# Kernel tuning notes

Hardware: AMD Instinct MI355X
Metric: run time of the kernel (lower is better)

The kernel has to match this reference:

```python
import jax, jax.numpy as jnp
import numpy as np

I, H, O, L = 256, 512, 256, 2
B, S = 64, 512


def setup_inputs() -> dict:
    key = jax.random.key(0)
    ks = jax.random.split(key, 10)
    s_in = 1.0 / np.sqrt(I)
    s_h = 1.0 / np.sqrt(H)
    return {
        "x": jax.random.normal(ks[0], (B, S, I), dtype=jnp.float32),
        "h_prev": jnp.zeros((L, B, H), dtype=jnp.float32),
        "W_in": jax.random.uniform(ks[1], (I, H), jnp.float32, -s_in, s_in),
        "b_in": jax.random.uniform(ks[2], (H,), jnp.float32, -s_in, s_in),
        "W_i2h": jax.random.uniform(ks[3], (L, H, H), jnp.float32, -s_h, s_h),
        "b_i2h": jax.random.uniform(ks[4], (L, H), jnp.float32, -s_h, s_h),
        "W_h2h": jax.random.uniform(ks[5], (L, H, H), jnp.float32, -s_h, s_h),
        "b_h2h": jax.random.uniform(ks[6], (L, H), jnp.float32, -s_h, s_h),
        "W_out": jax.random.uniform(ks[7], (H, O), jnp.float32, -s_h, s_h),
        "b_out": jax.random.uniform(ks[8], (O,), jnp.float32, -s_h, s_h),
    }


def reference(x, h_prev, W_in, b_in, W_i2h, b_i2h, W_h2h, b_h2h, W_out, b_out):
    # x: [B, S, I]; h_prev: [L, B, H]
    def step(h, x_t):  # h: [L,B,H], x_t: [B,I]
        layer_in = x_t @ W_in + b_in  # [B,H]
        new_hs = []
        for l in range(L):
            h_l = jnp.tanh(layer_in @ W_i2h[l] + b_i2h[l] + h[l] @ W_h2h[l] + b_h2h[l])
            new_hs.append(h_l)
            layer_in = h_l
        h_new = jnp.stack(new_hs, axis=0)  # [L,B,H]
        out_t = layer_in @ W_out + b_out  # [B,O]
        return h_new, out_t

    xs = jnp.swapaxes(x, 0, 1)  # [S,B,I]
    h_t, outs = jax.lax.scan(step, h_prev, xs)
    outputs = jnp.swapaxes(outs, 0, 1)  # [B,S,O]
    return outputs, h_t
```

## Files before the change

### kernel.cpp

```cpp
#include <hip/hip_runtime.h>
#include <math.h>


constexpr int BB = 64;
constexpr int SS = 512;
constexpr int II = 256;
constexpr int HH = 512;
constexpr int OO = 256;
constexpr int BH = BB * HH;
constexpr int RING_D = 4;
constexpr int STR0 = 772;
constexpr int STR1 = 1028;
constexpr int PSTR = 36;
constexpr int HREG = 8 * STR1;
constexpr int PREG = 8 * 32 * PSTR;
constexpr int LDS_BYTES = (HREG + PREG) * 4;

#define SCOPE_AGENT __HIP_MEMORY_SCOPE_AGENT

__device__ __forceinline__ unsigned ld_flag(const unsigned* p) {
    return __hip_atomic_load((unsigned*)p, __ATOMIC_RELAXED, SCOPE_AGENT);
}
__device__ __forceinline__ void add_flag(unsigned* p) {
    __hip_atomic_fetch_add(p, 1u, __ATOMIC_RELAXED, SCOPE_AGENT);
}
__device__ __forceinline__ void wait_ge(const unsigned* p, unsigned target) {
    while (ld_flag(p) < target) __builtin_amdgcn_s_sleep(1);
}

union F2U { float2 f; unsigned long long u; };
__device__ __forceinline__ float2 ld_coh2(const float* p) {
    F2U v;
    v.u = __hip_atomic_load((unsigned long long*)p, __ATOMIC_RELAXED, SCOPE_AGENT);
    return v.f;
}
__device__ __forceinline__ void st_coh1(float* p, float a) {
    __hip_atomic_store(p, a, __ATOMIC_RELAXED, SCOPE_AGENT);
}

template <int N>
__device__ __forceinline__ void pin4(float4 (&w)[N]) {
    #pragma unroll
    for (int i = 0; i < N; ++i)
        asm volatile("" : "+v"(w[i].x), "+v"(w[i].y), "+v"(w[i].z), "+v"(w[i].w));
}

__global__ __launch_bounds__(256) void fold_k(
    const float* __restrict__ Win, const float* __restrict__ bin,
    const float* __restrict__ Wi2h, const float* __restrict__ bi2h,
    const float* __restrict__ bh2h,
    float* __restrict__ W0, float* __restrict__ b0)
{
    int gid = blockIdx.x * 256 + threadIdx.x;
    const float* Wi0 = Wi2h;
    if (gid < II * HH) {
        int i = gid / HH, j = gid % HH;
        float acc = 0.f;
        for (int k = 0; k < HH; ++k)
            acc = fmaf(Win[i * HH + k], Wi0[k * HH + j], acc);
        W0[gid] = acc;
    } else if (gid < II * HH + HH) {
        int j = gid - II * HH;
        float acc = bi2h[j] + bh2h[j];
        for (int k = 0; k < HH; ++k)
            acc = fmaf(bin[k], Wi0[k * HH + j], acc);
        b0[j] = acc;
    }
}

template <int LAYER>
__device__ __forceinline__ void rnn_body(
    const float* __restrict__ x, const float* __restrict__ hprev,
    const float* __restrict__ Wi2h, const float* __restrict__ bi2h,
    const float* __restrict__ Wh2h, const float* __restrict__ bh2h,
    const float* __restrict__ W0, const float* __restrict__ b0,
    float* __restrict__ ring, float* __restrict__ H1,
    unsigned* __restrict__ c0, unsigned* __restrict__ c1,
    float* hbuf, float* pbuf)
{
    constexpr int NJ  = LAYER ? 8 : 6;
    constexpr int STR = LAYER ? STR1 : STR0;

    const int tid  = threadIdx.x;
    const int id   = blockIdx.x & 127;
    const int rg   = id >> 4;
    const int cg   = id & 15;
    const int row0 = rg * 8;
    const int col0 = cg * 32;
    const int kg   = tid & 31;
    const int cgrp = (tid >> 5) & 7;
    const int cbase = col0 + cgrp * 4;

    float4 w4[NJ * 4];
    #pragma unroll
    for (int j = 0; j < NJ; ++j) {
        #pragma unroll
        for (int e = 0; e < 4; ++e) {
            int k = j * 128 + kg * 4 + e;
            const float* src;
            if (LAYER == 0)
                src = (k < 512) ? (Wh2h + (size_t)k * HH + cbase)
                                : (W0 + (size_t)(k - 512) * HH + cbase);
            else
                src = (k < 512) ? (Wi2h + (size_t)HH * HH + (size_t)k * HH + cbase)
                                : (Wh2h + (size_t)HH * HH + (size_t)(k - 512) * HH + cbase);
            w4[j * 4 + e] = *(const float4*)src;
        }
    }
    pin4(w4);

    float bias_red;
    {
        int c = col0 + (tid & 31);
        bias_red = LAYER ? (bi2h[HH + c] + bh2h[HH + c]) : b0[c];
    }
    const int rr = tid >> 5, cl = tid & 31;

    for (int t = 0; t < SS; ++t) {
        if (tid == 0) {
            if (LAYER == 0) {
                if (t >= 1) wait_ge(c0 + rg, 16u * (unsigned)t);
                if (t >= RING_D) wait_ge(c1 + rg, 16u * (unsigned)(t - RING_D + 1));
            } else {
                wait_ge(c0 + rg, 16u * (unsigned)(t + 1));
                if (t >= 1) wait_ge(c1 + rg, 16u * (unsigned)t);
            }
        }
        __syncthreads();

        if (LAYER == 0) {
            const float* hsrc = (t == 0)
                ? (hprev + (size_t)row0 * HH)
                : (ring + (size_t)((t - 1) & (RING_D - 1)) * BH + (size_t)row0 * HH);
            float2 tmp[8];
            #pragma unroll
            for (int u = 0; u < 8; ++u) tmp[u] = ld_coh2(hsrc + u * HH + 2 * tid);
            float4 xv[2];
            #pragma unroll
            for (int v = 0; v < 2; ++v) {
                int rx = 4 * v + (tid >> 6);
                xv[v] = *(const float4*)(x + ((size_t)(row0 + rx) * SS + t) * II + 4 * (tid & 63));
            }
            #pragma unroll
            for (int u = 0; u < 8; ++u) *(float2*)&hbuf[u * STR + 2 * tid] = tmp[u];
            #pragma unroll
            for (int v = 0; v < 2; ++v) {
                int rx = 4 * v + (tid >> 6);
                *(float4*)&hbuf[rx * STR + 512 + 4 * (tid & 63)] = xv[v];
            }
        } else {
            const float* h0src = ring + (size_t)(t & (RING_D - 1)) * BH + (size_t)row0 * HH;
            const float* h1src = (t == 0)
                ? (hprev + BH + (size_t)row0 * HH)
                : (H1 + (size_t)(t - 1) * BH + (size_t)row0 * HH);
            float2 ta[8], tb[8];
            #pragma unroll
            for (int u = 0; u < 8; ++u) ta[u] = ld_coh2(h0src + u * HH + 2 * tid);
            #pragma unroll
            for (int u = 0; u < 8; ++u) tb[u] = ld_coh2(h1src + u * HH + 2 * tid);
            #pragma unroll
            for (int u = 0; u < 8; ++u) *(float2*)&hbuf[u * STR + 2 * tid] = ta[u];
            #pragma unroll
            for (int u = 0; u < 8; ++u) *(float2*)&hbuf[u * STR + 512 + 2 * tid] = tb[u];
        }
        __syncthreads();

        float4 acc[8];
        #pragma unroll
        for (int r = 0; r < 8; ++r) acc[r] = make_float4(0.f, 0.f, 0.f, 0.f);
        #pragma unroll
        for (int r = 0; r < 8; ++r) {
            #pragma unroll
            for (int j = 0; j < NJ; ++j) {
                float4 h4 = *(const float4*)&hbuf[r * STR + j * 128 + kg * 4];
                float4 wa = w4[j * 4 + 0];
                float4 wb = w4[j * 4 + 1];
                float4 wc = w4[j * 4 + 2];
                float4 wd = w4[j * 4 + 3];
                acc[r].x = fmaf(h4.x, wa.x, acc[r].x);
                acc[r].y = fmaf(h4.x, wa.y, acc[r].y);
                acc[r].z = fmaf(h4.x, wa.z, acc[r].z);
                acc[r].w = fmaf(h4.x, wa.w, acc[r].w);
                acc[r].x = fmaf(h4.y, wb.x, acc[r].x);
                acc[r].y = fmaf(h4.y, wb.y, acc[r].y);
                acc[r].z = fmaf(h4.y, wb.z, acc[r].z);
                acc[r].w = fmaf(h4.y, wb.w, acc[r].w);
                acc[r].x = fmaf(h4.z, wc.x, acc[r].x);
                acc[r].y = fmaf(h4.z, wc.y, acc[r].y);
                acc[r].z = fmaf(h4.z, wc.z, acc[r].z);
                acc[r].w = fmaf(h4.z, wc.w, acc[r].w);
                acc[r].x = fmaf(h4.w, wd.x, acc[r].x);
                acc[r].y = fmaf(h4.w, wd.y, acc[r].y);
                acc[r].z = fmaf(h4.w, wd.z, acc[r].z);
                acc[r].w = fmaf(h4.w, wd.w, acc[r].w);
            }
        }

        #pragma unroll
        for (int r = 0; r < 8; ++r) {
            pbuf[(r * 32 + cgrp * 4 + 0) * PSTR + kg] = acc[r].x;
            pbuf[(r * 32 + cgrp * 4 + 1) * PSTR + kg] = acc[r].y;
            pbuf[(r * 32 + cgrp * 4 + 2) * PSTR + kg] = acc[r].z;
            pbuf[(r * 32 + cgrp * 4 + 3) * PSTR + kg] = acc[r].w;
        }
        __syncthreads();
        {
            float s = 0.f;
            #pragma unroll
            for (int j2 = 0; j2 < 8; ++j2) {
                float4 v = *(const float4*)&pbuf[(rr * 32 + cl) * PSTR + 4 * j2];
                s += (v.x + v.y) + (v.z + v.w);
            }
            float o = tanhf(s + bias_red);
            float* dst = LAYER
                ? (H1 + (size_t)t * BH + (size_t)(row0 + rr) * HH + col0 + cl)
                : (ring + (size_t)(t & (RING_D - 1)) * BH + (size_t)(row0 + rr) * HH + col0 + cl);
            st_coh1(dst, o);
        }
        __syncthreads();
        if (tid == 0) add_flag((LAYER ? c1 : c0) + rg);
    }
}

__global__ __launch_bounds__(256, 1) void rnn_seq6(
    const float* __restrict__ x, const float* __restrict__ hprev,
    const float* __restrict__ Wi2h, const float* __restrict__ bi2h,
    const float* __restrict__ Wh2h, const float* __restrict__ bh2h,
    const float* __restrict__ W0, const float* __restrict__ b0,
    float* __restrict__ ring, float* __restrict__ H1,
    unsigned* __restrict__ c0, unsigned* __restrict__ c1)
{
    extern __shared__ float lds[];
    float* hbuf = lds;
    float* pbuf = lds + HREG;
    if (blockIdx.x >> 7)
        rnn_body<1>(x, hprev, Wi2h, bi2h, Wh2h, bh2h, W0, b0, ring, H1, c0, c1, hbuf, pbuf);
    else
        rnn_body<0>(x, hprev, Wi2h, bi2h, Wh2h, bh2h, W0, b0, ring, H1, c0, c1, hbuf, pbuf);
}

__global__ __launch_bounds__(256) void out_k(
    const float* __restrict__ H1, const float* __restrict__ Wout,
    const float* __restrict__ bout, float* __restrict__ out)
{
    __shared__ float wchunk[32 * 256];
    __shared__ float htile[16 * 32];
    const int tid = threadIdx.x;
    const int r0 = blockIdx.x * 16;

    float acc[16];
    #pragma unroll
    for (int mm = 0; mm < 16; ++mm) acc[mm] = 0.f;

    for (int kc = 0; kc < HH; kc += 32) {
        for (int idx = tid; idx < 32 * 256; idx += 256)
            wchunk[idx] = Wout[(size_t)(kc + (idx >> 8)) * OO + (idx & 255)];
        for (int idx = tid; idx < 16 * 32; idx += 256) {
            int mm = idx >> 5, kk = idx & 31;
            htile[idx] = H1[(size_t)(r0 + mm) * HH + kc + kk];
        }
        __syncthreads();
        for (int kk = 0; kk < 32; ++kk) {
            float w = wchunk[kk * 256 + tid];
            #pragma unroll
            for (int mm = 0; mm < 16; ++mm)
                acc[mm] = fmaf(htile[mm * 32 + kk], w, acc[mm]);
        }
        __syncthreads();
    }
    float bo = bout[tid];
    #pragma unroll
    for (int mm = 0; mm < 16; ++mm) {
        int rr = r0 + mm;
        int s = rr >> 6, b = rr & 63;
        out[((size_t)b * SS + s) * OO + tid] = acc[mm] + bo;
    }
}

__global__ __launch_bounds__(256) void tail_k(
    const float* __restrict__ ring, const float* __restrict__ H1,
    float* __restrict__ out_tail)
{
    int gid = blockIdx.x * 256 + threadIdx.x;
    if (gid < BB * HH)
        out_tail[gid] = ring[((SS - 1) & (RING_D - 1)) * BH + gid];
    else if (gid < 2 * BB * HH)
        out_tail[gid] = H1[(size_t)(SS - 1) * BH + (gid - BB * HH)];
}

extern "C" void kernel_launch(void* const* d_in, const int* in_sizes, int n_in,
                              void* d_out, int out_size, void* d_ws, size_t ws_size,
                              hipStream_t stream)
{
    const float* x     = (const float*)d_in[0];
    const float* hprev = (const float*)d_in[1];
    const float* Win   = (const float*)d_in[2];
    const float* bin   = (const float*)d_in[3];
    const float* Wi2h  = (const float*)d_in[4];
    const float* bi2h  = (const float*)d_in[5];
    const float* Wh2h  = (const float*)d_in[6];
    const float* bh2h  = (const float*)d_in[7];
    const float* Wout  = (const float*)d_in[8];
    const float* bout  = (const float*)d_in[9];

    float* ws   = (float*)d_ws;
    float* W0   = ws;
    float* b0   = W0 + (size_t)II * HH;
    float* ring = b0 + HH;
    float* H1   = ring + (size_t)RING_D * BH;
    unsigned* cnt = (unsigned*)(H1 + (size_t)SS * BH);
    unsigned* c0 = cnt;
    unsigned* c1 = cnt + 8;
    float* out  = (float*)d_out;

    hipMemsetAsync(cnt, 0, 16 * sizeof(unsigned), stream);
    fold_k<<<dim3((II * HH + HH + 255) / 256), dim3(256), 0, stream>>>(
        Win, bin, Wi2h, bi2h, bh2h, W0, b0);
    hipFuncSetAttribute((const void*)rnn_seq6,
                        hipFuncAttributeMaxDynamicSharedMemorySize, LDS_BYTES);
    rnn_seq6<<<dim3(256), dim3(256), LDS_BYTES, stream>>>(
        x, hprev, Wi2h, bi2h, Wh2h, bh2h, W0, b0, ring, H1, c0, c1);
    out_k<<<dim3(BB * SS / 16), dim3(256), 0, stream>>>(H1, Wout, bout, out);
    tail_k<<<dim3((2 * BB * HH) / 256), dim3(256), 0, stream>>>(
        ring, H1, out + (size_t)BB * SS * OO);
}
```

Before: 6.075 ms.

## Replace counter barriers with tagged hidden-state words and stream weights from memory

The per-row-group step counters are replaced by an 8-bit step tag packed into the low mantissa bits of each stored hidden value. Consumers spin on the data words themselves until every tag matches, so the separate flag round-trip is gone and the ring shrinks to double buffers per layer. Layer 1 now writes twice per step: a tagged copy into its ring and an untagged copy into H1. Weights are no longer pinned in registers but reloaded from global memory inside the inner FMA loop, which adds memory traffic each step and costs a little precision in the recurrent state.

Measured after the change: 5.112 ms. 15.8% less time.

```diff
diff --git a/kernel.cpp b/kernel.cpp
--- a/kernel.cpp
+++ b/kernel.cpp
@@ -8,7 +8,6 @@
 constexpr int HH = 512;
 constexpr int OO = 256;
 constexpr int BH = BB * HH;
-constexpr int RING_D = 4;
 constexpr int STR0 = 772;
 constexpr int STR1 = 1028;
 constexpr int PSTR = 36;
@@ -27,22 +26,17 @@
 __device__ __forceinline__ void wait_ge(const unsigned* p, unsigned target) {
     while (ld_flag(p) < target) __builtin_amdgcn_s_sleep(1);
 }
-
-union F2U { float2 f; unsigned long long u; };
-__device__ __forceinline__ float2 ld_coh2(const float* p) {
-    F2U v;
-    v.u = __hip_atomic_load((unsigned long long*)p, __ATOMIC_RELAXED, SCOPE_AGENT);
-    return v.f;
+__device__ __forceinline__ float ld_coh1(const float* p) {
+    return __hip_atomic_load((float*)p, __ATOMIC_RELAXED, SCOPE_AGENT);
 }
 __device__ __forceinline__ void st_coh1(float* p, float a) {
     __hip_atomic_store(p, a, __ATOMIC_RELAXED, SCOPE_AGENT);
 }
-
-template <int N>
-__device__ __forceinline__ void pin4(float4 (&w)[N]) {
-    #pragma unroll
-    for (int i = 0; i < N; ++i)
-        asm volatile("" : "+v"(w[i].x), "+v"(w[i].y), "+v"(w[i].z), "+v"(w[i].w));
+__device__ __forceinline__ float tagf(float v, unsigned t8) {
+    return __uint_as_float((__float_as_uint(v) & 0xFFFFFF00u) | t8);
+}
+__device__ __forceinline__ bool tag_ok(float v, unsigned t8) {
+    return (__float_as_uint(v) & 255u) == t8;
 }
 
 __global__ __launch_bounds__(256) void fold_k(
@@ -74,8 +68,8 @@
     const float* __restrict__ Wi2h, const float* __restrict__ bi2h,
     const float* __restrict__ Wh2h, const float* __restrict__ bh2h,
     const float* __restrict__ W0, const float* __restrict__ b0,
-    float* __restrict__ ring, float* __restrict__ H1,
-    unsigned* __restrict__ c0, unsigned* __restrict__ c1,
+    float* __restrict__ h0ring, float* __restrict__ h1ring,
+    float* __restrict__ H1, unsigned* __restrict__ c1,
     float* hbuf, float* pbuf)
 {
     constexpr int NJ  = LAYER ? 8 : 6;
@@ -91,24 +85,6 @@
     const int cgrp = (tid >> 5) & 7;
     const int cbase = col0 + cgrp * 4;
 
-    float4 w4[NJ * 4];
-    #pragma unroll
-    for (int j = 0; j < NJ; ++j) {
-        #pragma unroll
-        for (int e = 0; e < 4; ++e) {
-            int k = j * 128 + kg * 4 + e;
-            const float* src;
-            if (LAYER == 0)
-                src = (k < 512) ? (Wh2h + (size_t)k * HH + cbase)
-                                : (W0 + (size_t)(k - 512) * HH + cbase);
-            else
-                src = (k < 512) ? (Wi2h + (size_t)HH * HH + (size_t)k * HH + cbase)
-                                : (Wh2h + (size_t)HH * HH + (size_t)(k - 512) * HH + cbase);
-            w4[j * 4 + e] = *(const float4*)src;
-        }
-    }
-    pin4(w4);
-
     float bias_red;
     {
         int c = col0 + (tid & 31);
@@ -117,51 +93,105 @@
     const int rr = tid >> 5, cl = tid & 31;
 
     for (int t = 0; t < SS; ++t) {
-        if (tid == 0) {
-            if (LAYER == 0) {
-                if (t >= 1) wait_ge(c0 + rg, 16u * (unsigned)t);
-                if (t >= RING_D) wait_ge(c1 + rg, 16u * (unsigned)(t - RING_D + 1));
+        if (LAYER == 0 && t >= 2 && tid == 0)
+            wait_ge(c1 + rg, 16u * (unsigned)(t - 1));
+        __syncthreads();
+
+        if (LAYER == 0) {
+            if (t == 0) {
+                float2 tmp[8];
+                #pragma unroll
+                for (int u = 0; u < 8; ++u)
+                    tmp[u] = *(const float2*)(hprev + (size_t)(row0 + u) * HH + 2 * tid);
+                #pragma unroll
+                for (int u = 0; u < 8; ++u)
+                    *(float2*)&hbuf[u * STR + 2 * tid] = tmp[u];
             } else {
-                wait_ge(c0 + rg, 16u * (unsigned)(t + 1));
-                if (t >= 1) wait_ge(c1 + rg, 16u * (unsigned)t);
-            }
-        }
-        __syncthreads();
-
-        if (LAYER == 0) {
-            const float* hsrc = (t == 0)
-                ? (hprev + (size_t)row0 * HH)
-                : (ring + (size_t)((t - 1) & (RING_D - 1)) * BH + (size_t)row0 * HH);
-            float2 tmp[8];
-            #pragma unroll
-            for (int u = 0; u < 8; ++u) tmp[u] = ld_coh2(hsrc + u * HH + 2 * tid);
+                const float* rs = h0ring + (size_t)((t - 1) & 1) * BH + (size_t)row0 * HH;
+                const unsigned tg = (unsigned)(t & 255);
+                float v[16];
+                for (;;) {
+                    bool ok = true;
+                    #pragma unroll
+                    for (int u = 0; u < 8; ++u) {
+                        v[2 * u + 0] = ld_coh1(rs + u * HH + tid);
+                        v[2 * u + 1] = ld_coh1(rs + u * HH + 256 + tid);
+                    }
+                    #pragma unroll
+                    for (int e = 0; e < 16; ++e) ok &= tag_ok(v[e], tg);
+                    if (ok) break;
+                    __builtin_amdgcn_s_sleep(1);
+                }
+                #pragma unroll
+                for (int u = 0; u < 8; ++u) {
+                    hbuf[u * STR + tid]       = v[2 * u + 0];
+                    hbuf[u * STR + 256 + tid] = v[2 * u + 1];
+                }
+            }
             float4 xv[2];
             #pragma unroll
-            for (int v = 0; v < 2; ++v) {
-                int rx = 4 * v + (tid >> 6);
-                xv[v] = *(const float4*)(x + ((size_t)(row0 + rx) * SS + t) * II + 4 * (tid & 63));
-            }
-            #pragma unroll
-            for (int u = 0; u < 8; ++u) *(float2*)&hbuf[u * STR + 2 * tid] = tmp[u];
-            #pragma unroll
-            for (int v = 0; v < 2; ++v) {
-                int rx = 4 * v + (tid >> 6);
-                *(float4*)&hbuf[rx * STR + 512 + 4 * (tid & 63)] = xv[v];
+            for (int w = 0; w < 2; ++w) {
+                int rx = 4 * w + (tid >> 6);
+                xv[w] = *(const float4*)(x + ((size_t)(row0 + rx) * SS + t) * II + 4 * (tid & 63));
+            }
+            #pragma unroll
+            for (int w = 0; w < 2; ++w) {
+                int rx = 4 * w + (tid >> 6);
+                *(float4*)&hbuf[rx * STR + 512 + 4 * (tid & 63)] = xv[w];
             }
         } else {
-            const float* h0src = ring + (size_t)(t & (RING_D - 1)) * BH + (size_t)row0 * HH;
-            const float* h1src = (t == 0)
-                ? (hprev + BH + (size_t)row0 * HH)
-                : (H1 + (size_t)(t - 1) * BH + (size_t)row0 * HH);
-            float2 ta[8], tb[8];
-            #pragma unroll
-            for (int u = 0; u < 8; ++u) ta[u] = ld_coh2(h0src + u * HH + 2 * tid);
-            #pragma unroll
-            for (int u = 0; u < 8; ++u) tb[u] = ld_coh2(h1src + u * HH + 2 * tid);
-            #pragma unroll
-            for (int u = 0; u < 8; ++u) *(float2*)&hbuf[u * STR + 2 * tid] = ta[u];
-            #pragma unroll
-            for (int u = 0; u < 8; ++u) *(float2*)&hbuf[u * STR + 512 + 2 * tid] = tb[u];
+            if (t == 0) {
+                float2 tmp[8];
+                #pragma unroll
+                for (int u = 0; u < 8; ++u)
+                    tmp[u] = *(const float2*)(hprev + BH + (size_t)(row0 + u) * HH + 2 * tid);
+                #pragma unroll
+                for (int u = 0; u < 8; ++u)
+                    *(float2*)&hbuf[u * STR + 512 + 2 * tid] = tmp[u];
+            } else {
+                const float* rs = h1ring + (size_t)((t - 1) & 1) * BH + (size_t)row0 * HH;
+                const unsigned tg = (unsigned)(t & 255);
+                float v[16];
+                for (;;) {
+                    bool ok = true;
+                    #pragma unroll
+                    for (int u = 0; u < 8; ++u) {
+                        v[2 * u + 0] = ld_coh1(rs + u * HH + tid);
+                        v[2 * u + 1] = ld_coh1(rs + u * HH + 256 + tid);
+                    }
+                    #pragma unroll
+                    for (int e = 0; e < 16; ++e) ok &= tag_ok(v[e], tg);
+                    if (ok) break;
+                    __builtin_amdgcn_s_sleep(1);
+                }
+                #pragma unroll
+                for (int u = 0; u < 8; ++u) {
+                    hbuf[u * STR + 512 + tid]       = v[2 * u + 0];
+                    hbuf[u * STR + 512 + 256 + tid] = v[2 * u + 1];
+                }
+            }
+            {
+                const float* rs = h0ring + (size_t)(t & 1) * BH + (size_t)row0 * HH;
+                const unsigned tg = (unsigned)((t + 1) & 255);
+                float v[16];
+                for (;;) {
+                    bool ok = true;
+                    #pragma unroll
+                    for (int u = 0; u < 8; ++u) {
+                        v[2 * u + 0] = ld_coh1(rs + u * HH + tid);
+                        v[2 * u + 1] = ld_coh1(rs + u * HH + 256 + tid);
+                    }
+                    #pragma unroll
+                    for (int e = 0; e < 16; ++e) ok &= tag_ok(v[e], tg);
+                    if (ok) break;
+                    __builtin_amdgcn_s_sleep(1);
+                }
+                #pragma unroll
+                for (int u = 0; u < 8; ++u) {
+                    hbuf[u * STR + tid]       = v[2 * u + 0];
+                    hbuf[u * STR + 256 + tid] = v[2 * u + 1];
+                }
+            }
         }
         __syncthreads();
 
@@ -172,11 +202,19 @@
         for (int r = 0; r < 8; ++r) {
             #pragma unroll
             for (int j = 0; j < NJ; ++j) {
-                float4 h4 = *(const float4*)&hbuf[r * STR + j * 128 + kg * 4];
-                float4 wa = w4[j * 4 + 0];
-                float4 wb = w4[j * 4 + 1];
-                float4 wc = w4[j * 4 + 2];
-                float4 wd = w4[j * 4 + 3];
+                int k = j * 128 + kg * 4;
+                const float* wsrc;
+                if (LAYER == 0)
+                    wsrc = (k < 512) ? (Wh2h + (size_t)k * HH + cbase)
+                                     : (W0 + (size_t)(k - 512) * HH + cbase);
+                else
+                    wsrc = (k < 512) ? (Wi2h + (size_t)HH * HH + (size_t)k * HH + cbase)
+                                     : (Wh2h + (size_t)HH * HH + (size_t)(k - 512) * HH + cbase);
+                float4 h4 = *(const float4*)&hbuf[r * STR + k];
+                float4 wa = *(const float4*)(wsrc);
+                float4 wb = *(const float4*)(wsrc + HH);
+                float4 wc = *(const float4*)(wsrc + 2 * HH);
+                float4 wd = *(const float4*)(wsrc + 3 * HH);
                 acc[r].x = fmaf(h4.x, wa.x, acc[r].x);
                 acc[r].y = fmaf(h4.x, wa.y, acc[r].y);
                 acc[r].z = fmaf(h4.x, wa.z, acc[r].z);
@@ -212,31 +250,38 @@
                 s += (v.x + v.y) + (v.z + v.w);
             }
             float o = tanhf(s + bias_red);
-            float* dst = LAYER
-                ? (H1 + (size_t)t * BH + (size_t)(row0 + rr) * HH + col0 + cl)
-                : (ring + (size_t)(t & (RING_D - 1)) * BH + (size_t)(row0 + rr) * HH + col0 + cl);
-            st_coh1(dst, o);
-        }
-        __syncthreads();
-        if (tid == 0) add_flag((LAYER ? c1 : c0) + rg);
-    }
-}
-
-__global__ __launch_bounds__(256, 1) void rnn_seq6(
+            const unsigned myt8 = (unsigned)((t + 1) & 255);
+            if (LAYER == 0) {
+                st_coh1(h0ring + (size_t)(t & 1) * BH + (size_t)(row0 + rr) * HH + col0 + cl,
+                        tagf(o, myt8));
+            } else {
+                st_coh1(h1ring + (size_t)(t & 1) * BH + (size_t)(row0 + rr) * HH + col0 + cl,
+                        tagf(o, myt8));
+                H1[(size_t)t * BH + (size_t)(row0 + rr) * HH + col0 + cl] = o;
+            }
+        }
+        __syncthreads();
+        if (LAYER == 1 && tid == 0) add_flag(c1 + rg);
+    }
+}
+
+__global__ __launch_bounds__(256, 1) void rnn_seq7(
     const float* __restrict__ x, const float* __restrict__ hprev,
     const float* __restrict__ Wi2h, const float* __restrict__ bi2h,
     const float* __restrict__ Wh2h, const float* __restrict__ bh2h,
     const float* __restrict__ W0, const float* __restrict__ b0,
-    float* __restrict__ ring, float* __restrict__ H1,
-    unsigned* __restrict__ c0, unsigned* __restrict__ c1)
+    float* __restrict__ h0ring, float* __restrict__ h1ring,
+    float* __restrict__ H1, unsigned* __restrict__ c1)
 {
     extern __shared__ float lds[];
     float* hbuf = lds;
     float* pbuf = lds + HREG;
     if (blockIdx.x >> 7)
-        rnn_body<1>(x, hprev, Wi2h, bi2h, Wh2h, bh2h, W0, b0, ring, H1, c0, c1, hbuf, pbuf);
+        rnn_body<1>(x, hprev, Wi2h, bi2h, Wh2h, bh2h, W0, b0,
+                    h0ring, h1ring, H1, c1, hbuf, pbuf);
     else
-        rnn_body<0>(x, hprev, Wi2h, bi2h, Wh2h, bh2h, W0, b0, ring, H1, c0, c1, hbuf, pbuf);
+        rnn_body<0>(x, hprev, Wi2h, bi2h, Wh2h, bh2h, W0, b0,
+                    h0ring, h1ring, H1, c1, hbuf, pbuf);
 }
 
 __global__ __launch_bounds__(256) void out_k(
@@ -278,12 +323,12 @@
 }
 
 __global__ __launch_bounds__(256) void tail_k(
-    const float* __restrict__ ring, const float* __restrict__ H1,
+    const float* __restrict__ h0ring, const float* __restrict__ H1,
     float* __restrict__ out_tail)
 {
     int gid = blockIdx.x * 256 + threadIdx.x;
     if (gid < BB * HH)
-        out_tail[gid] = ring[((SS - 1) & (RING_D - 1)) * BH + gid];
+        out_tail[gid] = h0ring[(size_t)((SS - 1) & 1) * BH + gid];
     else if (gid < 2 * BB * HH)
         out_tail[gid] = H1[(size_t)(SS - 1) * BH + (gid - BB * HH)];
 }
@@ -303,24 +348,23 @@
     const float* Wout  = (const float*)d_in[8];
     const float* bout  = (const float*)d_in[9];
 
-    float* ws   = (float*)d_ws;
-    float* W0   = ws;
-    float* b0   = W0 + (size_t)II * HH;
-    float* ring = b0 + HH;
-    float* H1   = ring + (size_t)RING_D * BH;
-    unsigned* cnt = (unsigned*)(H1 + (size_t)SS * BH);
-    unsigned* c0 = cnt;
-    unsigned* c1 = cnt + 8;
-    float* out  = (float*)d_out;
-
-    hipMemsetAsync(cnt, 0, 16 * sizeof(unsigned), stream);
+    float* ws     = (float*)d_ws;
+    float* W0     = ws;
+    float* b0     = W0 + (size_t)II * HH;
+    float* h0ring = b0 + HH;
+    float* h1ring = h0ring + 2 * (size_t)BH;
+    float* H1     = h1ring + 2 * (size_t)BH;
+    unsigned* c1  = (unsigned*)(H1 + (size_t)SS * BH);
+    float* out    = (float*)d_out;
+
+    hipMemsetAsync(c1, 0, 16 * sizeof(unsigned), stream);
     fold_k<<<dim3((II * HH + HH + 255) / 256), dim3(256), 0, stream>>>(
         Win, bin, Wi2h, bi2h, bh2h, W0, b0);
-    hipFuncSetAttribute((const void*)rnn_seq6,
+    hipFuncSetAttribute((const void*)rnn_seq7,
                         hipFuncAttributeMaxDynamicSharedMemorySize, LDS_BYTES);
-    rnn_seq6<<<dim3(256), dim3(256), LDS_BYTES, stream>>>(
-        x, hprev, Wi2h, bi2h, Wh2h, bh2h, W0, b0, ring, H1, c0, c1);
+    rnn_seq7<<<dim3(256), dim3(256), LDS_BYTES, stream>>>(
+        x, hprev, Wi2h, bi2h, Wh2h, bh2h, W0, b0, h0ring, h1ring, H1, c1);
     out_k<<<dim3(BB * SS / 16), dim3(256), 0, stream>>>(H1, Wout, bout, out);
     tail_k<<<dim3((2 * BB * HH) / 256), dim3(256), 0, stream>>>(
-        ring, H1, out + (size_t)BB * SS * OO);
-}
+        h0ring, H1, out + (size_t)BB * SS * OO);
+}
```
